# Optimization experiments

Hardware: AMD Instinct MI355X
Metric: run time of the kernel (lower is better)

The kernel has to match this reference:

```python
import jax, jax.numpy as jnp
import numpy as np

HEADS = 8


def setup_inputs() -> dict:
    key = jax.random.key(0)
    ks = jax.random.split(key, 18)
    B, L, D, N = 512, 70, 128, 100000
    r = lambda i, shape: jax.random.normal(ks[i], shape, dtype=jnp.float32) * 0.1
    return {
        "hidden": r(0, (B, L, D)),
        "hidden0": r(1, (B, L, D)),
        "mask": jnp.ones((B, L), dtype=jnp.int32),
        "s": r(2, (B, D)),
        "emb": r(3, (N, D)),
        "attn_in_w": r(4, (3 * D, D)),
        "attn_in_b": r(5, (3 * D,)),
        "attn_out_w": r(6, (D, D)),
        "attn_out_b": r(7, (D,)),
        "w_zero": r(8, (D, D)),
        "b_zero": r(9, (D,)),
        "w_one": r(10, (D, D)),
        "b_one": r(11, (D,)),
        "w_two": r(12, (D, D)),
        "b_two": r(13, (D,)),
        "w_three": r(14, (HEADS, D)),
        "w_gate": r(15, (1, 2 * D)),
        "w_trans": r(16, (D, 2 * D)),
        "b_trans": r(17, (D,)),
    }


def _mha(q, k, v, in_w, in_b, out_w, out_b, h):
    # torch.nn.MultiheadAttention, eval mode (dropout=0)
    B, Lq, D = q.shape
    Lk = k.shape[1]
    hd = D // h
    wq, wk, wv = jnp.split(in_w, 3, axis=0)
    bq, bk, bv = jnp.split(in_b, 3)
    qp = (q @ wq.T + bq).reshape(B, Lq, h, hd)
    kp = (k @ wk.T + bk).reshape(B, Lk, h, hd)
    vp = (v @ wv.T + bv).reshape(B, Lk, h, hd)
    scores = jnp.einsum("bqhd,bkhd->bhqk", qp, kp) / jnp.sqrt(jnp.float32(hd))
    w = jax.nn.softmax(scores, axis=-1)
    o = jnp.einsum("bhqk,bkhd->bqhd", w, vp).reshape(B, Lq, D)
    return o @ out_w.T + out_b


def reference(hidden, hidden0, mask, s, emb,
              attn_in_w, attn_in_b, attn_out_w, attn_out_b,
              w_zero, b_zero, w_one, b_one, w_two, b_two,
              w_three, w_gate, w_trans, b_trans):
    B, L, D = hidden.shape
    H = HEADS
    # last-item gather (last_k = 1)
    last_idx = jnp.clip(jnp.sum(mask, axis=1) - 1, 0, 1000)
    ht0 = hidden[jnp.arange(B), last_idx]  # [B, D]
    ht1 = ht0
    # attention of pooled session vector over item states
    ht = _mha(s[:, None, :], hidden, hidden,
              attn_in_w, attn_in_b, attn_out_w, attn_out_b, H)  # [B, 1, D]
    # sigmoid gated fusion of hidden0 / hidden
    sigma = jax.nn.sigmoid(jnp.concatenate([hidden0, hidden], axis=-1) @ w_gate.T)  # [B, L, 1]
    hidden = hidden0 * sigma + hidden * (1.0 - sigma)
    # additive multi-head attention scores
    q0 = (ht1 @ w_zero.T + b_zero)[:, None, :]          # [B, 1, D]
    q1 = ht @ w_one.T + b_one                           # [B, 1, D]
    q2 = hidden @ w_two.T + b_two                       # [B, L, D]
    alpha = jax.nn.sigmoid(q1 + q2 + q0) @ w_three.T    # [B, L, H]
    alpha = jnp.where((mask == 0)[:, :, None], -jnp.inf, alpha)
    alpha = jax.nn.softmax(alpha, axis=1)
    # head-split mask-weighted sum reduction
    mf = mask.astype(hidden.dtype)[:, :, None]
    a = jnp.sum((alpha[..., None] * hidden.reshape(B, L, H, D // H)).reshape(B, L, D) * mf, axis=1)  # [B, D]
    # hybrid transform with last item
    a = jnp.concatenate([a, ht0], axis=1) @ w_trans.T + b_trans
    # normalized scoring against item table (skipping padding idx 0)
    b = emb[1:]
    a = a / (jnp.linalg.norm(a, axis=1, keepdims=True) + 1e-12)
    b = b / (jnp.linalg.norm(b, axis=1, keepdims=True) + 1e-12)
    scores = 12.0 * (a @ b.T)  # [B, n_node-1]
    return scores
```

## Files before the change

### kernel.cpp

```cpp
#include <hip/hip_runtime.h>
#include <hip/hip_bf16.h>

#define B_SZ 512
#define L_SZ 70
#define D_SZ 128
#define NCOL 99999
#define M_ROWS (B_SZ * L_SZ)

typedef __attribute__((ext_vector_type(4))) float f32x4;
typedef __attribute__((ext_vector_type(8))) short bf16x8;

static __device__ __forceinline__ short f2bf(float x) {
    union { float f; unsigned u; } v; v.f = x;
    unsigned r = v.u + 0x7fffu + ((v.u >> 16) & 1u);
    return (short)(r >> 16);
}
static __device__ __forceinline__ float bf2f(unsigned short h) {
    union { unsigned u; float f; } v; v.u = ((unsigned)h) << 16; return v.f;
}

__global__ void k_prep(const float* attn_in_w, const float* w_two,
                       const float* attn_out_w, const float* w_zero,
                       const float* w_one, const float* w_trans,
                       short* Wkv, short* W2,
                       float* wqT, float* woT, float* w0T, float* w1T, float* wtT) {
    int i = blockIdx.x * 256 + threadIdx.x;
    if (i < 256 * 128) Wkv[i] = f2bf(attn_in_w[128 * 128 + i]);
    if (i < 128 * 128) {
        W2[i] = f2bf(w_two[i]);
        int r = i >> 7, c = i & 127;
        wqT[c * 128 + r] = attn_in_w[i];
        woT[c * 128 + r] = attn_out_w[i];
        w0T[c * 128 + r] = w_zero[i];
        w1T[c * 128 + r] = w_one[i];
    }
    if (i < 128 * 256) {
        int r = i >> 8, c = i & 255;
        wtT[c * 128 + r] = w_trans[i];
    }
}

__global__ void k_gate(const float* hidden, const float* hidden0,
                       const float* w_gate, short* g_bf) {
    int row = blockIdx.x, t = threadIdx.x;
    float h0 = hidden0[row * 128 + t], h = hidden[row * 128 + t];
    float p = h0 * w_gate[t] + h * w_gate[128 + t];
    for (int off = 32; off; off >>= 1) p += __shfl_down(p, off);
    __shared__ float part[2];
    __shared__ float sig_sh;
    if ((t & 63) == 0) part[t >> 6] = p;
    __syncthreads();
    if (t == 0) {
        float tot = part[0] + part[1];
        sig_sh = 1.f / (1.f + __expf(-tot));
    }
    __syncthreads();
    float sg = sig_sh;
    g_bf[row * 128 + t] = f2bf(h0 * sg + h * (1.f - sg));
}

__global__ void k_gemm_kv(const float* hidden, const short* Wkv,
                          const float* attn_in_b, short* kv) {
    int lane = threadIdx.x & 63, w = threadIdx.x >> 6;
    int r0 = blockIdx.x * 64 + w * 16;
    int ar = r0 + (lane & 15);
    int kbase = (lane >> 4) * 8;
    bf16x8 aF[4];
    const float* Arow = hidden + ar * 128 + kbase;
    for (int kk = 0; kk < 4; kk++) {
        float4 x0 = *(const float4*)(Arow + kk * 32);
        float4 x1 = *(const float4*)(Arow + kk * 32 + 4);
        bf16x8 f;
        f[0] = f2bf(x0.x); f[1] = f2bf(x0.y); f[2] = f2bf(x0.z); f[3] = f2bf(x0.w);
        f[4] = f2bf(x1.x); f[5] = f2bf(x1.y); f[6] = f2bf(x1.z); f[7] = f2bf(x1.w);
        aF[kk] = f;
    }
    int cl = lane & 15;
    int rowbase = r0 + (lane >> 4) * 4;
    for (int ct = 0; ct < 16; ct++) {
        int c = ct * 16 + cl;
        f32x4 acc = {0.f, 0.f, 0.f, 0.f};
        const short* Brow = Wkv + c * 128 + kbase;
        for (int kk = 0; kk < 4; kk++) {
            bf16x8 bF = *(const bf16x8*)(Brow + kk * 32);
            acc = __builtin_amdgcn_mfma_f32_16x16x32_bf16(aF[kk], bF, acc, 0, 0, 0);
        }
        float bias = attn_in_b[128 + c];
        for (int rg = 0; rg < 4; rg++)
            kv[(rowbase + rg) * 256 + c] = f2bf(acc[rg] + bias);
    }
}

__global__ void k_attn(const float* hidden, const int* mask, const float* s,
                       const float* wqT, const float* attn_in_b,
                       const short* kv,
                       const float* woT, const float* attn_out_b,
                       const float* w0T, const float* b_zero,
                       const float* w1T, const float* b_one,
                       float* ht0, float* q01) {
    int b = blockIdx.x, t = threadIdx.x;
    __shared__ float kp_s[L_SZ][128];
    __shared__ float s_sh[128], qp_s[128], o_s[128], ht_s[128], ht0_s[128];
    __shared__ float sc[8][72];
    __shared__ int idx_sh;
    if (t < 64) {
        int acc = 0;
        for (int l = t; l < L_SZ; l += 64) acc += mask[b * L_SZ + l];
        for (int off = 32; off; off >>= 1) acc += __shfl_down(acc, off);
        if (t == 0) {
            int idx = acc - 1;
            if (idx < 0) idx = 0;
            if (idx > L_SZ - 1) idx = L_SZ - 1;
            idx_sh = idx;
        }
    }
    s_sh[t] = s[b * 128 + t];
    const unsigned short* kvrow = (const unsigned short*)kv + (size_t)b * L_SZ * 256;
    for (int i = t; i < L_SZ * 128; i += 128) {
        int l = i >> 7, d = i & 127;
        kp_s[l][d] = bf2f(kvrow[l * 256 + d]);
    }
    __syncthreads();
    {
        float h0 = hidden[((size_t)b * L_SZ + idx_sh) * 128 + t];
        ht0[b * 128 + t] = h0;
        ht0_s[t] = h0;
        float acc = attn_in_b[t];
        for (int k = 0; k < 128; k++) acc += s_sh[k] * wqT[k * 128 + t];
        qp_s[t] = acc;
    }
    __syncthreads();
    for (int task = t; task < 8 * L_SZ; task += 128) {
        int h = task / L_SZ, l = task % L_SZ;
        float acc = 0.f;
        for (int j = 0; j < 16; j++) acc += qp_s[h * 16 + j] * kp_s[l][h * 16 + j];
        sc[h][l] = acc * 0.25f;
    }
    __syncthreads();
    if (t < 8) {
        float m = -1e30f;
        for (int l = 0; l < L_SZ; l++) m = fmaxf(m, sc[t][l]);
        float ssum = 0.f;
        for (int l = 0; l < L_SZ; l++) { float e = __expf(sc[t][l] - m); sc[t][l] = e; ssum += e; }
        float inv = 1.f / ssum;
        for (int l = 0; l < L_SZ; l++) sc[t][l] *= inv;
    }
    __syncthreads();
    {
        int h = t >> 4;
        float acc = 0.f;
        for (int l = 0; l < L_SZ; l++) acc += sc[h][l] * bf2f(kvrow[l * 256 + 128 + t]);
        o_s[t] = acc;
    }
    __syncthreads();
    {
        float acc = attn_out_b[t];
        for (int k = 0; k < 128; k++) acc += o_s[k] * woT[k * 128 + t];
        ht_s[t] = acc;
    }
    __syncthreads();
    {
        float acc = b_one[t] + b_zero[t];
        for (int k = 0; k < 128; k++) acc += ht_s[k] * w1T[k * 128 + t] + ht0_s[k] * w0T[k * 128 + t];
        q01[b * 128 + t] = acc;
    }
}

__global__ void k_gemm_q2_alpha(const short* g_bf, const short* W2, const float* b_two,
                                const float* q01, const float* w_three, float* alphaL) {
    int lane = threadIdx.x & 63, w = threadIdx.x >> 6;
    int r0 = blockIdx.x * 64 + w * 16;
    int ar = r0 + (lane & 15);
    int kbase = (lane >> 4) * 8;
    bf16x8 aF[4];
    const short* Arow = g_bf + ar * 128 + kbase;
    for (int kk = 0; kk < 4; kk++) aF[kk] = *(const bf16x8*)(Arow + kk * 32);
    float part[4][8];
    for (int r = 0; r < 4; r++)
        for (int h = 0; h < 8; h++) part[r][h] = 0.f;
    int cl = lane & 15;
    int rowbase = r0 + (lane >> 4) * 4;
    for (int ct = 0; ct < 8; ct++) {
        int c = ct * 16 + cl;
        f32x4 acc = {0.f, 0.f, 0.f, 0.f};
        const short* Brow = W2 + c * 128 + kbase;
        for (int kk = 0; kk < 4; kk++) {
            bf16x8 bF = *(const bf16x8*)(Brow + kk * 32);
            acc = __builtin_amdgcn_mfma_f32_16x16x32_bf16(aF[kk], bF, acc, 0, 0, 0);
        }
        float bias = b_two[c];
        for (int rg = 0; rg < 4; rg++) {
            int row = rowbase + rg;
            int bb = row / L_SZ;
            float val = acc[rg] + bias + q01[bb * 128 + c];
            float sg = 1.f / (1.f + __expf(-val));
            for (int h = 0; h < 8; h++) part[rg][h] += sg * w_three[h * 128 + c];
        }
    }
    for (int off = 1; off < 16; off <<= 1)
        for (int rg = 0; rg < 4; rg++)
            for (int h = 0; h < 8; h++)
                part[rg][h] += __shfl_xor(part[rg][h], off);
    if ((lane & 15) == 0) {
        for (int rg = 0; rg < 4; rg++) {
            int row = rowbase + rg;
            for (int h = 0; h < 8; h++) alphaL[row * 8 + h] = part[rg][h];
        }
    }
}

__global__ void k_alpha_a(const float* alphaL, const int* mask, const short* g_bf,
                          const float* ht0, const float* wtT, const float* b_trans,
                          short* a_bf) {
    int b = blockIdx.x, t = threadIdx.x;
    __shared__ float aw[L_SZ][8];
    __shared__ float mf[L_SZ];
    __shared__ float a_s[128];
    __shared__ float ht0_s[128];
    __shared__ float red[2];
    for (int i = t; i < L_SZ; i += 128) mf[i] = (float)mask[b * L_SZ + i];
    for (int i = t; i < L_SZ * 8; i += 128) aw[i >> 3][i & 7] = alphaL[b * L_SZ * 8 + i];
    ht0_s[t] = ht0[b * 128 + t];
    __syncthreads();
    if (t < 8) {
        float m = -1e30f;
        for (int l = 0; l < L_SZ; l++) {
            float v = (mf[l] == 0.f) ? -1e30f : aw[l][t];
            if (v > m) m = v;
        }
        float ssum = 0.f;
        for (int l = 0; l < L_SZ; l++) {
            float v = (mf[l] == 0.f) ? -1e30f : aw[l][t];
            float e = __expf(v - m);
            ssum += e; aw[l][t] = e;
        }
        float inv = 1.f / ssum;
        for (int l = 0; l < L_SZ; l++) aw[l][t] *= inv;
    }
    __syncthreads();
    int h = t >> 4;
    float acc = 0.f;
    const unsigned short* grow = (const unsigned short*)g_bf + b * L_SZ * 128 + t;
    for (int l = 0; l < L_SZ; l++) acc += aw[l][h] * bf2f(grow[l * 128]) * mf[l];
    a_s[t] = acc;
    __syncthreads();
    float a2 = b_trans[t];
    for (int k = 0; k < 128; k++)
        a2 += a_s[k] * wtT[k * 128 + t] + ht0_s[k] * wtT[(128 + k) * 128 + t];
    float sq = a2 * a2;
    for (int off = 32; off; off >>= 1) sq += __shfl_down(sq, off);
    if ((t & 63) == 0) red[t >> 6] = sq;
    __syncthreads();
    float nrm = sqrtf(red[0] + red[1]) + 1e-12f;
    a_bf[b * 128 + t] = f2bf(a2 / nrm);
}

__global__ void __launch_bounds__(256, 4) k_final(const short* a_bf, const float* emb, float* out) {
    __shared__ float lds_c[16][132];
    int t = threadIdx.x;
    int lane = t & 63, w = t >> 6;
    int bx = blockIdx.x;
    int cl = lane & 15, kg = lane >> 4;
    int kbase = kg * 8;

    bf16x8 bF[2][4];
    for (int ct2 = 0; ct2 < 2; ct2++) {
        int c0 = bx * 128 + w * 32 + ct2 * 16 + cl;
        float x[4][8];
        float ss = 0.f;
        if (c0 < NCOL) {
            const float* e = emb + (size_t)(c0 + 1) * 128 + kbase;
            for (int kk = 0; kk < 4; kk++) {
                float4 v0 = *(const float4*)(e + kk * 32);
                float4 v1 = *(const float4*)(e + kk * 32 + 4);
                x[kk][0] = v0.x; x[kk][1] = v0.y; x[kk][2] = v0.z; x[kk][3] = v0.w;
                x[kk][4] = v1.x; x[kk][5] = v1.y; x[kk][6] = v1.z; x[kk][7] = v1.w;
                for (int j = 0; j < 8; j++) ss += x[kk][j] * x[kk][j];
            }
        } else {
            for (int kk = 0; kk < 4; kk++)
                for (int j = 0; j < 8; j++) x[kk][j] = 0.f;
        }
        ss += __shfl_xor(ss, 16);
        ss += __shfl_xor(ss, 32);
        float inv = 1.f / (sqrtf(ss) + 1e-12f);
        for (int kk = 0; kk < 4; kk++) {
            bf16x8 f;
            for (int j = 0; j < 8; j++) f[j] = f2bf(x[kk][j] * inv);
            bF[ct2][kk] = f;
        }
    }

    int cend = NCOL - bx * 128;
    if (cend > 128) cend = 128;

    for (int rt = 0; rt < 32; rt++) {
        bf16x8 aF[4];
        const short* Arow = a_bf + ((size_t)(rt * 16 + cl)) * 128 + kbase;
        for (int kk = 0; kk < 4; kk++) aF[kk] = *(const bf16x8*)(Arow + kk * 32);
        f32x4 acc0 = {0.f, 0.f, 0.f, 0.f}, acc1 = {0.f, 0.f, 0.f, 0.f};
        for (int kk = 0; kk < 4; kk++) {
            acc0 = __builtin_amdgcn_mfma_f32_16x16x32_bf16(aF[kk], bF[0][kk], acc0, 0, 0, 0);
            acc1 = __builtin_amdgcn_mfma_f32_16x16x32_bf16(aF[kk], bF[1][kk], acc1, 0, 0, 0);
        }
        __syncthreads();
        for (int rg = 0; rg < 4; rg++) {
            lds_c[kg * 4 + rg][w * 32 + cl]      = 12.f * acc0[rg];
            lds_c[kg * 4 + rg][w * 32 + 16 + cl] = 12.f * acc1[rg];
        }
        __syncthreads();
        for (int p = 0; p < 4; p++) {
            int row = p * 4 + w;
            size_t gr = (size_t)(rt * 16 + row) * NCOL + (size_t)bx * 128;
            for (int q = 0; q < 2; q++) {
                int col = q * 64 + lane;
                if (col < cend) out[gr + col] = lds_c[row][col];
            }
        }
    }
}

extern "C" void kernel_launch(void* const* d_in, const int* in_sizes, int n_in,
                              void* d_out, int out_size, void* d_ws, size_t ws_size,
                              hipStream_t stream) {
    const float* hidden     = (const float*)d_in[0];
    const float* hidden0    = (const float*)d_in[1];
    const int*   mask       = (const int*)d_in[2];
    const float* s          = (const float*)d_in[3];
    const float* emb        = (const float*)d_in[4];
    const float* attn_in_w  = (const float*)d_in[5];
    const float* attn_in_b  = (const float*)d_in[6];
    const float* attn_out_w = (const float*)d_in[7];
    const float* attn_out_b = (const float*)d_in[8];
    const float* w_zero     = (const float*)d_in[9];
    const float* b_zero     = (const float*)d_in[10];
    const float* w_one      = (const float*)d_in[11];
    const float* b_one      = (const float*)d_in[12];
    const float* w_two      = (const float*)d_in[13];
    const float* b_two      = (const float*)d_in[14];
    const float* w_three    = (const float*)d_in[15];
    const float* w_gate     = (const float*)d_in[16];
    const float* w_trans    = (const float*)d_in[17];
    const float* b_trans    = (const float*)d_in[18];
    float* out = (float*)d_out;

    char* p = (char*)d_ws;
    float* ht0    = (float*)p; p += (size_t)B_SZ * 128 * 4;
    float* q01    = (float*)p; p += (size_t)B_SZ * 128 * 4;
    float* alphaL = (float*)p; p += (size_t)B_SZ * L_SZ * 8 * 4;
    short* a_bf   = (short*)p; p += (size_t)B_SZ * 128 * 2;
    short* Wkv    = (short*)p; p += (size_t)256 * 128 * 2;
    short* W2     = (short*)p; p += (size_t)128 * 128 * 2;
    float* wqT    = (float*)p; p += (size_t)128 * 128 * 4;
    float* woT    = (float*)p; p += (size_t)128 * 128 * 4;
    float* w0T    = (float*)p; p += (size_t)128 * 128 * 4;
    float* w1T    = (float*)p; p += (size_t)128 * 128 * 4;
    float* wtT    = (float*)p; p += (size_t)256 * 128 * 4;
    short* g_bf   = (short*)p; p += (size_t)M_ROWS * 128 * 2;
    short* kv     = (short*)p; p += (size_t)M_ROWS * 256 * 2;

    k_prep<<<128, 256, 0, stream>>>(attn_in_w, w_two, attn_out_w, w_zero, w_one, w_trans,
                                    Wkv, W2, wqT, woT, w0T, w1T, wtT);
    k_gate<<<M_ROWS, 128, 0, stream>>>(hidden, hidden0, w_gate, g_bf);
    k_gemm_kv<<<M_ROWS / 64, 256, 0, stream>>>(hidden, Wkv, attn_in_b, kv);
    k_attn<<<B_SZ, 128, 0, stream>>>(hidden, mask, s, wqT, attn_in_b, kv,
                                     woT, attn_out_b, w0T, b_zero, w1T, b_one, ht0, q01);
    k_gemm_q2_alpha<<<M_ROWS / 64, 256, 0, stream>>>(g_bf, W2, b_two, q01, w_three, alphaL);
    k_alpha_a<<<B_SZ, 128, 0, stream>>>(alphaL, mask, g_bf, ht0, wtT, b_trans, a_bf);
    k_final<<<(NCOL + 127) / 128, 256, 0, stream>>>(a_bf, emb, out);
}
```

Baseline: 459.5 us.

## Fuse gate and KV projection kernels; per-wave vectorized output stores in final GEMM

```diff
diff --git a/kernel.cpp b/kernel.cpp
--- a/kernel.cpp
+++ b/kernel.cpp
@@ -9,6 +9,8 @@
 
 typedef __attribute__((ext_vector_type(4))) float f32x4;
 typedef __attribute__((ext_vector_type(8))) short bf16x8;
+typedef __attribute__((ext_vector_type(4))) short s16x4;
+typedef __attribute__((ext_vector_type(8))) unsigned short u16x8;
 
 static __device__ __forceinline__ short f2bf(float x) {
     union { float f; unsigned u; } v; v.f = x;
@@ -40,43 +42,54 @@
     }
 }
 
-__global__ void k_gate(const float* hidden, const float* hidden0,
-                       const float* w_gate, short* g_bf) {
-    int row = blockIdx.x, t = threadIdx.x;
-    float h0 = hidden0[row * 128 + t], h = hidden[row * 128 + t];
-    float p = h0 * w_gate[t] + h * w_gate[128 + t];
-    for (int off = 32; off; off >>= 1) p += __shfl_down(p, off);
-    __shared__ float part[2];
-    __shared__ float sig_sh;
-    if ((t & 63) == 0) part[t >> 6] = p;
-    __syncthreads();
-    if (t == 0) {
-        float tot = part[0] + part[1];
-        sig_sh = 1.f / (1.f + __expf(-tot));
-    }
-    __syncthreads();
-    float sg = sig_sh;
-    g_bf[row * 128 + t] = f2bf(h0 * sg + h * (1.f - sg));
-}
-
-__global__ void k_gemm_kv(const float* hidden, const short* Wkv,
-                          const float* attn_in_b, short* kv) {
-    int lane = threadIdx.x & 63, w = threadIdx.x >> 6;
-    int r0 = blockIdx.x * 64 + w * 16;
-    int ar = r0 + (lane & 15);
-    int kbase = (lane >> 4) * 8;
+__global__ void k_gatekv(const float* hidden, const float* hidden0, const float* w_gate,
+                         const short* Wkv, const float* attn_in_b,
+                         short* g_bf, short* kv) {
+    __shared__ float wg[256];
+    __shared__ short h_lds[64][136];
+    int t = threadIdx.x;
+    int r0 = blockIdx.x * 64;
+    wg[t] = w_gate[t];
+    int row = t >> 2, q = t & 3;
+    const float* hrow  = hidden  + (size_t)(r0 + row) * 128;
+    const float* h0row = hidden0 + (size_t)(r0 + row) * 128;
+    float h[32], h0[32];
+    for (int i = 0; i < 8; i++) {
+        float4 a = *(const float4*)(hrow  + i * 16 + q * 4);
+        float4 b = *(const float4*)(h0row + i * 16 + q * 4);
+        h[i*4+0]=a.x; h[i*4+1]=a.y; h[i*4+2]=a.z; h[i*4+3]=a.w;
+        h0[i*4+0]=b.x; h0[i*4+1]=b.y; h0[i*4+2]=b.z; h0[i*4+3]=b.w;
+    }
+    __syncthreads();
+    float p = 0.f;
+    for (int i = 0; i < 8; i++)
+        for (int j = 0; j < 4; j++) {
+            int c = i * 16 + q * 4 + j;
+            p += h0[i*4+j] * wg[c] + h[i*4+j] * wg[128 + c];
+        }
+    p += __shfl_xor(p, 1);
+    p += __shfl_xor(p, 2);
+    float sg = 1.f / (1.f + __expf(-p));
+    float om = 1.f - sg;
+    for (int i = 0; i < 8; i++) {
+        s16x4 gv, hv;
+        for (int j = 0; j < 4; j++) {
+            gv[j] = f2bf(h0[i*4+j] * sg + h[i*4+j] * om);
+            hv[j] = f2bf(h[i*4+j]);
+        }
+        int c = i * 16 + q * 4;
+        *(s16x4*)(g_bf + (size_t)(r0 + row) * 128 + c) = gv;
+        *(s16x4*)(&h_lds[row][c]) = hv;
+    }
+    __syncthreads();
+    int lane = t & 63, w = t >> 6;
+    int arl = lane & 15, kg = lane >> 4;
+    int kbase = kg * 8;
     bf16x8 aF[4];
-    const float* Arow = hidden + ar * 128 + kbase;
-    for (int kk = 0; kk < 4; kk++) {
-        float4 x0 = *(const float4*)(Arow + kk * 32);
-        float4 x1 = *(const float4*)(Arow + kk * 32 + 4);
-        bf16x8 f;
-        f[0] = f2bf(x0.x); f[1] = f2bf(x0.y); f[2] = f2bf(x0.z); f[3] = f2bf(x0.w);
-        f[4] = f2bf(x1.x); f[5] = f2bf(x1.y); f[6] = f2bf(x1.z); f[7] = f2bf(x1.w);
-        aF[kk] = f;
-    }
+    for (int kk = 0; kk < 4; kk++)
+        aF[kk] = *(const bf16x8*)(&h_lds[w * 16 + arl][kbase + kk * 32]);
     int cl = lane & 15;
-    int rowbase = r0 + (lane >> 4) * 4;
+    int rowbase = r0 + w * 16 + kg * 4;
     for (int ct = 0; ct < 16; ct++) {
         int c = ct * 16 + cl;
         f32x4 acc = {0.f, 0.f, 0.f, 0.f};
@@ -87,7 +100,7 @@
         }
         float bias = attn_in_b[128 + c];
         for (int rg = 0; rg < 4; rg++)
-            kv[(rowbase + rg) * 256 + c] = f2bf(acc[rg] + bias);
+            kv[(size_t)(rowbase + rg) * 256 + c] = f2bf(acc[rg] + bias);
     }
 }
 
@@ -99,7 +112,7 @@
                        const float* w1T, const float* b_one,
                        float* ht0, float* q01) {
     int b = blockIdx.x, t = threadIdx.x;
-    __shared__ float kp_s[L_SZ][128];
+    __shared__ unsigned short kp_s[L_SZ][136];
     __shared__ float s_sh[128], qp_s[128], o_s[128], ht_s[128], ht0_s[128];
     __shared__ float sc[8][72];
     __shared__ int idx_sh;
@@ -118,7 +131,7 @@
     const unsigned short* kvrow = (const unsigned short*)kv + (size_t)b * L_SZ * 256;
     for (int i = t; i < L_SZ * 128; i += 128) {
         int l = i >> 7, d = i & 127;
-        kp_s[l][d] = bf2f(kvrow[l * 256 + d]);
+        kp_s[l][d] = kvrow[l * 256 + d];
     }
     __syncthreads();
     {
@@ -131,9 +144,12 @@
     }
     __syncthreads();
     for (int task = t; task < 8 * L_SZ; task += 128) {
-        int h = task / L_SZ, l = task % L_SZ;
+        int h = task / L_SZ, l = task - (task / L_SZ) * L_SZ;
+        const u16x8* kp = (const u16x8*)&kp_s[l][h * 16];
+        u16x8 k0 = kp[0], k1 = kp[1];
         float acc = 0.f;
-        for (int j = 0; j < 16; j++) acc += qp_s[h * 16 + j] * kp_s[l][h * 16 + j];
+        for (int j = 0; j < 8; j++)
+            acc += qp_s[h * 16 + j] * bf2f(k0[j]) + qp_s[h * 16 + 8 + j] * bf2f(k1[j]);
         sc[h][l] = acc * 0.25f;
     }
     __syncthreads();
@@ -256,7 +272,7 @@
 }
 
 __global__ void __launch_bounds__(256, 4) k_final(const short* a_bf, const float* emb, float* out) {
-    __shared__ float lds_c[16][132];
+    __shared__ float cbuf[4][16][36];
     int t = threadIdx.x;
     int lane = t & 63, w = t >> 6;
     int bx = blockIdx.x;
@@ -293,29 +309,33 @@
 
     int cend = NCOL - bx * 128;
     if (cend > 128) cend = 128;
+    int srow = lane >> 2, schunk = lane & 3;
+    int scb = w * 32 + schunk * 8;
 
     for (int rt = 0; rt < 32; rt++) {
         bf16x8 aF[4];
-        const short* Arow = a_bf + ((size_t)(rt * 16 + cl)) * 128 + kbase;
+        const short* Arow = a_bf + (size_t)(rt * 16 + cl) * 128 + kbase;
         for (int kk = 0; kk < 4; kk++) aF[kk] = *(const bf16x8*)(Arow + kk * 32);
         f32x4 acc0 = {0.f, 0.f, 0.f, 0.f}, acc1 = {0.f, 0.f, 0.f, 0.f};
         for (int kk = 0; kk < 4; kk++) {
             acc0 = __builtin_amdgcn_mfma_f32_16x16x32_bf16(aF[kk], bF[0][kk], acc0, 0, 0, 0);
             acc1 = __builtin_amdgcn_mfma_f32_16x16x32_bf16(aF[kk], bF[1][kk], acc1, 0, 0, 0);
         }
-        __syncthreads();
         for (int rg = 0; rg < 4; rg++) {
-            lds_c[kg * 4 + rg][w * 32 + cl]      = 12.f * acc0[rg];
-            lds_c[kg * 4 + rg][w * 32 + 16 + cl] = 12.f * acc1[rg];
-        }
-        __syncthreads();
-        for (int p = 0; p < 4; p++) {
-            int row = p * 4 + w;
-            size_t gr = (size_t)(rt * 16 + row) * NCOL + (size_t)bx * 128;
-            for (int q = 0; q < 2; q++) {
-                int col = q * 64 + lane;
-                if (col < cend) out[gr + col] = lds_c[row][col];
-            }
+            cbuf[w][kg * 4 + rg][cl]      = 12.f * acc0[rg];
+            cbuf[w][kg * 4 + rg][16 + cl] = 12.f * acc1[rg];
+        }
+        asm volatile("s_waitcnt lgkmcnt(0)" ::: "memory");
+        f32x4 v0 = *(const f32x4*)&cbuf[w][srow][schunk * 8];
+        f32x4 v1 = *(const f32x4*)&cbuf[w][srow][schunk * 8 + 4];
+        asm volatile("s_waitcnt lgkmcnt(0)" ::: "memory");
+        size_t gr = (size_t)(rt * 16 + srow) * NCOL + (size_t)bx * 128 + scb;
+        if (scb + 7 < cend) {
+            *(f32x4*)(out + gr) = v0;
+            *(f32x4*)(out + gr + 4) = v1;
+        } else {
+            for (int j = 0; j < 4; j++) if (scb + j < cend) out[gr + j] = v0[j];
+            for (int j = 0; j < 4; j++) if (scb + 4 + j < cend) out[gr + 4 + j] = v1[j];
         }
     }
 }
@@ -361,8 +381,8 @@
 
     k_prep<<<128, 256, 0, stream>>>(attn_in_w, w_two, attn_out_w, w_zero, w_one, w_trans,
                                     Wkv, W2, wqT, woT, w0T, w1T, wtT);
-    k_gate<<<M_ROWS, 128, 0, stream>>>(hidden, hidden0, w_gate, g_bf);
-    k_gemm_kv<<<M_ROWS / 64, 256, 0, stream>>>(hidden, Wkv, attn_in_b, kv);
+    k_gatekv<<<M_ROWS / 64, 256, 0, stream>>>(hidden, hidden0, w_gate, Wkv, attn_in_b,
+                                              g_bf, kv);
     k_attn<<<B_SZ, 128, 0, stream>>>(hidden, mask, s, wqT, attn_in_b, kv,
                                      woT, attn_out_b, w0T, b_zero, w1T, b_one, ht0, q01);
     k_gemm_q2_alpha<<<M_ROWS / 64, 256, 0, stream>>>(g_bf, W2, b_two, q01, w_three, alphaL);
```

Result: no change. 462.2 us (+0.6%).
